# Optimization experiments

Hardware: AMD Instinct MI355X
Metric: run time of the kernel (lower is better)

The kernel has to match this reference:

```python
import jax, jax.numpy as jnp
import numpy as np

N_NODES = 50000
N_EDGES = 800000
D_IN = 788
D_HID = 256
N_REL = 7
N_CLS = 2


def rgcn_conv(x, w_rel, w_root, b, src, dst, edge_type):
    """PyG RGCNConv with default mean aggregation per relation + root weight + bias.
    x: (N, F_in); w_rel: (R, F_in, F_out); w_root: (F_in, F_out); b: (F_out,).
    src/dst: (E,) with edge_index[0]=source j, edge_index[1]=target i.
    """
    R, _, F_out = w_rel.shape
    N = x.shape[0]
    # transform-then-gather (equivalent to PyG's gather-then-transform, cheaper)
    x_rel = jnp.einsum('nf,rfo->rno', x, w_rel)          # (R, N, F_out)
    msg = x_rel[edge_type, src]                           # (E, F_out)
    agg = jnp.zeros((R, N, F_out), x.dtype).at[edge_type, dst].add(msg)
    cnt = jnp.zeros((R, N), x.dtype).at[edge_type, dst].add(1.0)
    out = (agg / jnp.clip(cnt, 1.0)[..., None]).sum(0)    # mean per relation, summed over relations
    return out + x @ w_root + b


def setup_inputs() -> dict:
    key = jax.random.key(0)
    ks = jax.random.split(key, 9)
    x = jax.random.normal(ks[0], (N_NODES, D_IN), dtype=jnp.float32)
    edge_index = jax.random.randint(ks[1], (2, N_EDGES), 0, N_NODES, dtype=jnp.int64)
    edge_type = jax.random.randint(ks[2], (N_EDGES,), 0, N_REL, dtype=jnp.int64)
    s1 = 0.05
    w1_rel = jax.random.normal(ks[3], (N_REL, D_IN, D_HID), dtype=jnp.float32) * s1
    w1_root = jax.random.normal(ks[4], (D_IN, D_HID), dtype=jnp.float32) * s1
    b1 = jnp.zeros((D_HID,), dtype=jnp.float32)
    w2_rel = jax.random.normal(ks[5], (N_REL, D_HID, N_CLS), dtype=jnp.float32) * s1
    w2_root = jax.random.normal(ks[6], (D_HID, N_CLS), dtype=jnp.float32) * s1
    b2 = jnp.zeros((N_CLS,), dtype=jnp.float32)
    return {"x": x, "edge_index": edge_index, "edge_type": edge_type,
            "w1_rel": w1_rel, "w1_root": w1_root, "b1": b1,
            "w2_rel": w2_rel, "w2_root": w2_root, "b2": b2}


def reference(x, edge_index, edge_type, w1_rel, w1_root, b1, w2_rel, w2_root, b2):
    src, dst = edge_index[0], edge_index[1]
    h = jax.nn.relu(rgcn_conv(x, w1_rel, w1_root, b1, src, dst, edge_type))
    # F.dropout(p=0.5) is identity in eval mode
    out = rgcn_conv(h, w2_rel, w2_root, b2, src, dst, edge_type)
    return out
```

## Files before the change

### kernel.cpp

```cpp
#include <hip/hip_runtime.h>
#include <hip/hip_bf16.h>
#include <stdint.h>

#define N_NODES 50000
#define N_EDGES 800000
#define D_IN    788
#define D_INP   800
#define D_HID   256
#define N_REL   7
#define NBINS   (N_REL * N_NODES)
#define NSCANB  342
#define NXTILE  391

typedef __attribute__((ext_vector_type(8))) short bf16x8;
typedef __attribute__((ext_vector_type(4))) float f32x4;
typedef __attribute__((ext_vector_type(4))) unsigned int u32x4;

__device__ __forceinline__ unsigned short f2bf(float f) {
  union { __hip_bfloat16 h; unsigned short u; } v;
  v.h = __float2bfloat16(f);
  return v.u;
}

__device__ __forceinline__ f32x4 bf4(ushort4 g) {
  union { unsigned int u; float f; } a, b, c, d;
  a.u = (unsigned)g.x << 16; b.u = (unsigned)g.y << 16;
  c.u = (unsigned)g.z << 16; d.u = (unsigned)g.w << 16;
  return (f32x4){a.f, b.f, c.f, d.f};
}

#define GLOAD16(g, l) __builtin_amdgcn_global_load_lds(                      \
    (const __attribute__((address_space(1))) unsigned int*)(g),              \
    (__attribute__((address_space(3))) unsigned int*)(l), 16, 0, 0)

__global__ void k_conv_w(const float* __restrict__ w_rel, const float* __restrict__ w_root,
                         unsigned short* __restrict__ wt) {
  int t = blockIdx.x * blockDim.x + threadIdx.x;
  if (t >= 8 * D_HID * 100) return;
  int m = t / (D_HID * 100);
  int rem = t % (D_HID * 100);
  int o = rem / 100, gi = rem % 100;
  int chunk = gi >> 2, p = gi & 3;
  int g = p ^ ((o >> 1) & 3);
  int k0 = chunk * 32 + g * 8;
  const float* src = (m < N_REL) ? (w_rel + (size_t)m * D_IN * D_HID) : w_root;
  union { unsigned short us[8]; u32x4 v; } pk;
#pragma unroll
  for (int j = 0; j < 8; j++)
    pk.us[j] = (k0 + j < D_IN) ? f2bf(src[(size_t)(k0 + j) * D_HID + o]) : (unsigned short)0;
  *(u32x4*)(wt + (size_t)(m * D_HID + o) * D_INP + chunk * 32 + p * 8) = pk.v;
}

__global__ void k_xbf(const float* __restrict__ x, unsigned short* __restrict__ xb) {
  int t = blockIdx.x * blockDim.x + threadIdx.x;
  if (t >= N_NODES * 100) return;
  int n = t / 100, gi = t % 100;
  int chunk = gi >> 2, p = gi & 3;
  int g = p ^ ((n >> 1) & 3);
  int c = chunk * 32 + g * 8;
  union { unsigned short us[8]; u32x4 v; } pk;
  if (c + 7 < D_IN) {
    float4 a = *(const float4*)(x + (size_t)n * D_IN + c);
    float4 b = *(const float4*)(x + (size_t)n * D_IN + c + 4);
    pk.us[0] = f2bf(a.x); pk.us[1] = f2bf(a.y); pk.us[2] = f2bf(a.z); pk.us[3] = f2bf(a.w);
    pk.us[4] = f2bf(b.x); pk.us[5] = f2bf(b.y); pk.us[6] = f2bf(b.z); pk.us[7] = f2bf(b.w);
  } else {
#pragma unroll
    for (int j = 0; j < 8; j++)
      pk.us[j] = (c + j < D_IN) ? f2bf(x[(size_t)n * D_IN + c + j]) : (unsigned short)0;
  }
  *(u32x4*)(xb + (size_t)n * D_INP + chunk * 32 + p * 8) = pk.v;
}

__global__ void k_count(const int* __restrict__ etype, const int* __restrict__ edst,
                        int* __restrict__ cnt) {
  int t = blockIdx.x * blockDim.x + threadIdx.x;
  if (t >= N_EDGES) return;
  atomicAdd(&cnt[etype[t] * N_NODES + edst[t]], 1);
}

__global__ void k_scan1(const int* __restrict__ cnt, int* __restrict__ bsum) {
  __shared__ int wsh[4];
  int b = blockIdx.x, tid = threadIdx.x;
  int base = b * 1024 + tid * 4;
  int4 v = {0, 0, 0, 0};
  if (base + 3 < NBINS) v = *(const int4*)(cnt + base);
  else { for (int i = 0; i < 4; i++) if (base + i < NBINS) ((int*)&v)[i] = cnt[base + i]; }
  int s = v.x + v.y + v.z + v.w;
  for (int o = 32; o > 0; o >>= 1) s += __shfl_down(s, o);
  if ((tid & 63) == 0) wsh[tid >> 6] = s;
  __syncthreads();
  if (tid == 0) bsum[b] = wsh[0] + wsh[1] + wsh[2] + wsh[3];
}

__global__ void k_scan2(const int* __restrict__ bsum, int* __restrict__ boff) {
  __shared__ int tmp[512];
  int tid = threadIdx.x;
  int mine = (tid < NSCANB) ? bsum[tid] : 0;
  tmp[tid] = mine;
  __syncthreads();
  for (int o = 1; o < 512; o <<= 1) {
    int v = (tid >= o) ? tmp[tid - o] : 0;
    __syncthreads();
    tmp[tid] += v;
    __syncthreads();
  }
  if (tid < NSCANB) boff[tid] = tmp[tid] - mine;
}

__global__ void k_scan3(const int* __restrict__ cnt, const int* __restrict__ boff,
                        int* __restrict__ S) {
  __shared__ int wsum[4];
  int b = blockIdx.x, tid = threadIdx.x;
  int base = b * 1024 + tid * 4;
  int4 v = {0, 0, 0, 0};
  if (base + 3 < NBINS) v = *(const int4*)(cnt + base);
  else { for (int i = 0; i < 4; i++) if (base + i < NBINS) ((int*)&v)[i] = cnt[base + i]; }
  int s = v.x + v.y + v.z + v.w;
  int lane = tid & 63, w = tid >> 6;
  int sc = s;
  for (int o = 1; o < 64; o <<= 1) { int u = __shfl_up(sc, o); if (lane >= o) sc += u; }
  if (lane == 63) wsum[w] = sc;
  __syncthreads();
  int wbase = 0;
  for (int i = 0; i < w; i++) wbase += wsum[i];
  int excl = boff[b] + wbase + sc - s;
  int o0 = excl, o1 = excl + v.x, o2 = o1 + v.y, o3 = o2 + v.z;
  if (base + 3 < NBINS) { int4 o4 = {o0, o1, o2, o3}; *(int4*)(S + base) = o4; }
  else {
    if (base     < NBINS) S[base]     = o0;
    if (base + 1 < NBINS) S[base + 1] = o1;
    if (base + 2 < NBINS) S[base + 2] = o2;
    if (base + 3 < NBINS) S[base + 3] = o3;
  }
}

__global__ void k_scatter(const int* __restrict__ etype, const int* __restrict__ edst,
                          const int* __restrict__ esrc, const int* __restrict__ S,
                          int* __restrict__ rank, int* __restrict__ psrc) {
  int t = blockIdx.x * blockDim.x + threadIdx.x;
  if (t >= N_EDGES) return;
  int bin = etype[t] * N_NODES + edst[t];
  int r = atomicAdd(&rank[bin], 1);
  psrc[S[bin] + r] = esrc[t];
}

template<int SWZ, int NMAT>
__global__ __launch_bounds__(512) void k_gemm_g(
    const unsigned short* __restrict__ xb, const unsigned short* __restrict__ wt,
    unsigned short* __restrict__ xrs, int mb) {
  __shared__ __align__(16) unsigned short As[128 * 32];
  __shared__ __align__(16) unsigned short Bs[256 * 32];

  int tid = threadIdx.x;
  int bx, by;
  if (SWZ) {
    int b = blockIdx.x;
    int l = (b % 8) * (NXTILE * NMAT / 8) + b / 8;
    bx = l / NMAT; by = l % NMAT;
  } else {
    bx = blockIdx.x; by = blockIdx.y;
  }
  int mat = mb + by;
  int m0 = bx * 128;
  const unsigned short* wsec = wt + (size_t)mat * (D_HID * D_INP);
  int lane = tid & 63, w = tid >> 6;
  int wm = w >> 2, wn = w & 3;

  int ar = tid >> 2;
  int arow = m0 + ar; if (arow > N_NODES - 1) arow = N_NODES - 1;
  const unsigned short* asrc = xb + (size_t)arow * D_INP + (tid & 3) * 8;
  const unsigned short* bsrc0 = wsec + (size_t)(tid >> 2) * D_INP + (tid & 3) * 8;
  const unsigned short* bsrc1 = bsrc0 + (size_t)128 * D_INP;
  unsigned short* al = As + tid * 8;
  unsigned short* bl0 = Bs + tid * 8;
  unsigned short* bl1 = Bs + 4096 + tid * 8;

  f32x4 acc[4][4];
#pragma unroll
  for (int i = 0; i < 4; i++)
#pragma unroll
    for (int j = 0; j < 4; j++) acc[i][j] = (f32x4){0.f, 0.f, 0.f, 0.f};

  int row = lane & 15, quad = lane >> 4;
  int rg = (quad ^ ((row >> 1) & 3)) * 8;

  for (int ks = 0; ks < 25; ks++) {
    int ko = ks * 32;
    GLOAD16(asrc + ko, al);
    GLOAD16(bsrc0 + ko, bl0);
    GLOAD16(bsrc1 + ko, bl1);
    __syncthreads();

    bf16x8 af[4], bfr[4];
#pragma unroll
    for (int i = 0; i < 4; i++)
      af[i] = *(const bf16x8*)(As + (wm * 64 + i * 16 + row) * 32 + rg);
#pragma unroll
    for (int j = 0; j < 4; j++)
      bfr[j] = *(const bf16x8*)(Bs + (wn * 64 + j * 16 + row) * 32 + rg);
#pragma unroll
    for (int i = 0; i < 4; i++)
#pragma unroll
      for (int j = 0; j < 4; j++)
        acc[i][j] = __builtin_amdgcn_mfma_f32_16x16x32_bf16(af[i], bfr[j], acc[i][j], 0, 0, 0);
    __syncthreads();
  }

  int col_l = lane & 15, rquad = lane >> 4;
  unsigned short* xo = xrs + (size_t)by * ((size_t)N_NODES * D_HID);
#pragma unroll
  for (int i = 0; i < 4; i++) {
#pragma unroll
    for (int reg = 0; reg < 4; reg++) {
      int node = m0 + wm * 64 + i * 16 + rquad * 4 + reg;
      if (node < N_NODES) {
#pragma unroll
        for (int j = 0; j < 4; j++)
          xo[(size_t)node * D_HID + wn * 64 + j * 16 + col_l] = f2bf(acc[i][j][reg]);
      }
    }
  }
}

__global__ __launch_bounds__(256) void k_gemm_f(
    const float* __restrict__ x, const unsigned short* __restrict__ wt,
    unsigned short* __restrict__ xrs, int mb) {
  __shared__ __align__(16) unsigned short As[64 * 40];
  __shared__ __align__(16) unsigned short Bs[256 * 40];

  int tid = threadIdx.x;
  int mat = mb + blockIdx.y;
  int m0 = blockIdx.x * 64;
  const unsigned short* wsec = wt + (size_t)mat * (D_HID * D_INP);
  int lane = tid & 63, w = tid >> 6;

  int ra = tid >> 2, ca = tid & 3, ca8 = ca * 8;
  int arow = m0 + ra; if (arow > N_NODES - 1) arow = N_NODES - 1;
  const float* apf = x + (size_t)arow * D_IN;
  const unsigned short* bgp = wsec + (size_t)ra * D_INP + (ca ^ ((ra >> 1) & 3)) * 8;
  unsigned short* al = As + ra * 40 + ca8;
  unsigned short* bl = Bs + ra * 40 + ca8;

  f32x4 acc[4][4];
#pragma unroll
  for (int i = 0; i < 4; i++)
#pragma unroll
    for (int j = 0; j < 4; j++) acc[i][j] = (f32x4){0.f, 0.f, 0.f, 0.f};

  float4 pa0 = *(const float4*)(apf + ca8);
  float4 pa1 = *(const float4*)(apf + ca8 + 4);
  u32x4 pb0 = *(const u32x4*)(bgp);
  u32x4 pb1 = *(const u32x4*)(bgp +  64 * D_INP);
  u32x4 pb2 = *(const u32x4*)(bgp + 128 * D_INP);
  u32x4 pb3 = *(const u32x4*)(bgp + 192 * D_INP);

  int row = lane & 15, quad = lane >> 4;
  for (int ks = 0; ks < 25; ks++) {
    if (ks < 24) {
      union { unsigned short us[8]; u32x4 v; } pk;
      pk.us[0] = f2bf(pa0.x); pk.us[1] = f2bf(pa0.y);
      pk.us[2] = f2bf(pa0.z); pk.us[3] = f2bf(pa0.w);
      pk.us[4] = f2bf(pa1.x); pk.us[5] = f2bf(pa1.y);
      pk.us[6] = f2bf(pa1.z); pk.us[7] = f2bf(pa1.w);
      *(u32x4*)al = pk.v;
    } else {
      float v0 = pa0.x, v1 = pa0.y, v2 = pa0.z, v3 = pa0.w;
      float v4 = pa1.x, v5 = pa1.y, v6 = pa1.z, v7 = pa1.w;
      if (ca8 == 16) { v0 = pa1.x; v1 = pa1.y; v2 = pa1.z; v3 = pa1.w;
                       v4 = 0.f; v5 = 0.f; v6 = 0.f; v7 = 0.f; }
      if (ca8 == 24) { v0 = 0.f; v1 = 0.f; v2 = 0.f; v3 = 0.f;
                       v4 = 0.f; v5 = 0.f; v6 = 0.f; v7 = 0.f; }
      union { unsigned short us[8]; u32x4 v; } pk;
      pk.us[0] = f2bf(v0); pk.us[1] = f2bf(v1); pk.us[2] = f2bf(v2); pk.us[3] = f2bf(v3);
      pk.us[4] = f2bf(v4); pk.us[5] = f2bf(v5); pk.us[6] = f2bf(v6); pk.us[7] = f2bf(v7);
      *(u32x4*)al = pk.v;
    }
    *(u32x4*)bl = pb0;
    *(u32x4*)(bl +  64 * 40) = pb1;
    *(u32x4*)(bl + 128 * 40) = pb2;
    *(u32x4*)(bl + 192 * 40) = pb3;
    __syncthreads();

    if (ks < 24) {
      int on = (ks + 1) * 32 + ca8;
      int lo = (on > 780) ? 780 : on;
      pa0 = *(const float4*)(apf + lo);
      pa1 = *(const float4*)(apf + lo + 4);
      int ko = (ks + 1) * 32;
      pb0 = *(const u32x4*)(bgp + ko);
      pb1 = *(const u32x4*)(bgp + ko +  64 * D_INP);
      pb2 = *(const u32x4*)(bgp + ko + 128 * D_INP);
      pb3 = *(const u32x4*)(bgp + ko + 192 * D_INP);
    }

    bf16x8 af[4], bfr[4];
#pragma unroll
    for (int i = 0; i < 4; i++)
      af[i] = *(const bf16x8*)(As + (i * 16 + row) * 40 + quad * 8);
#pragma unroll
    for (int j = 0; j < 4; j++)
      bfr[j] = *(const bf16x8*)(Bs + (w * 64 + j * 16 + row) * 40 + quad * 8);
#pragma unroll
    for (int i = 0; i < 4; i++)
#pragma unroll
      for (int j = 0; j < 4; j++)
        acc[i][j] = __builtin_amdgcn_mfma_f32_16x16x32_bf16(af[i], bfr[j], acc[i][j], 0, 0, 0);
    __syncthreads();
  }

  int col_l = lane & 15, rquad = lane >> 4;
  unsigned short* xo = xrs + (size_t)blockIdx.y * ((size_t)N_NODES * D_HID);
#pragma unroll
  for (int i = 0; i < 4; i++) {
#pragma unroll
    for (int reg = 0; reg < 4; reg++) {
      int node = m0 + i * 16 + rquad * 4 + reg;
      if (node < N_NODES) {
#pragma unroll
        for (int j = 0; j < 4; j++)
          xo[(size_t)node * D_HID + w * 64 + j * 16 + col_l] = f2bf(acc[i][j][reg]);
      }
    }
  }
}

__global__ __launch_bounds__(256) void k_agg8(
    const unsigned short* __restrict__ xrs, const int* __restrict__ S,
    const int* __restrict__ cnt, const int* __restrict__ psrc,
    const float* __restrict__ b1, const float* __restrict__ w2rel,
    const float* __restrict__ w2root, float* __restrict__ y) {
  int n = blockIdx.x * 4 + (threadIdx.x >> 6);
  int lane = threadIdx.x & 63;
  if (n >= N_NODES) return;

  int c_l = 0, p_l = 0;
  if (lane < N_REL) {
    c_l = cnt[lane * N_NODES + n];
    p_l = S[lane * N_NODES + n];
  }

  f32x4 acc = (f32x4){0.f, 0.f, 0.f, 0.f};
#pragma unroll
  for (int r = 0; r < N_REL; r++) {
    int c = __shfl(c_l, r);
    if (c > 0) {
      int p = __shfl(p_l, r);
      const unsigned short* slab = xrs + (size_t)r * N_NODES * D_HID;
      f32x4 s = (f32x4){0.f, 0.f, 0.f, 0.f};
      int e = 0;
      for (; e + 1 < c; e += 2) {
        int s0 = psrc[p + e], s1 = psrc[p + e + 1];
        ushort4 g0 = *(const ushort4*)(slab + (size_t)s0 * D_HID + lane * 4);
        ushort4 g1 = *(const ushort4*)(slab + (size_t)s1 * D_HID + lane * 4);
        s += bf4(g0) + bf4(g1);
      }
      if (e < c) {
        int s0 = psrc[p + e];
        ushort4 g0 = *(const ushort4*)(slab + (size_t)s0 * D_HID + lane * 4);
        s += bf4(g0);
      }
      acc += s * (1.0f / (float)c);
    }
  }

  ushort4 gr = *(const ushort4*)(xrs + ((size_t)7 * N_NODES + n) * D_HID + lane * 4);
  acc += bf4(gr);
  f32x4 b = *(const f32x4*)(b1 + lane * 4);
  f32x4 hv;
  hv[0] = fmaxf(acc[0] + b[0], 0.f);
  hv[1] = fmaxf(acc[1] + b[1], 0.f);
  hv[2] = fmaxf(acc[2] + b[2], 0.f);
  hv[3] = fmaxf(acc[3] + b[3], 0.f);

#pragma unroll
  for (int m = 0; m < 8; m++) {
    const float* wp = (m < N_REL) ? (w2rel + m * (D_HID * 2)) : w2root;
    f32x4 wa = *(const f32x4*)(wp + lane * 8);
    f32x4 wb = *(const f32x4*)(wp + lane * 8 + 4);
    float d0 = hv[0] * wa[0] + hv[1] * wa[2] + hv[2] * wb[0] + hv[3] * wb[2];
    float d1 = hv[0] * wa[1] + hv[1] * wa[3] + hv[2] * wb[1] + hv[3] * wb[3];
#pragma unroll
    for (int off = 32; off > 0; off >>= 1) {
      d0 += __shfl_down(d0, off);
      d1 += __shfl_down(d1, off);
    }
    if (lane == 0) {
      y[(size_t)m * (N_NODES * 2) + n * 2]     = d0;
      y[(size_t)m * (N_NODES * 2) + n * 2 + 1] = d1;
    }
  }
}

__global__ __launch_bounds__(256) void k_agg(
    const unsigned short* __restrict__ xrs, const int* __restrict__ S,
    const int* __restrict__ cnt, const int* __restrict__ psrc,
    float* __restrict__ h, const float* __restrict__ b1,
    const float* __restrict__ w2rel, const float* __restrict__ w2root,
    float* __restrict__ y, int r0, int pass) {
  int n = blockIdx.x * 4 + (threadIdx.x >> 6);
  int lane = threadIdx.x & 63;
  if (n >= N_NODES) return;
  f32x4 acc;
  if (pass == 0) acc = (f32x4){0.f, 0.f, 0.f, 0.f};
  else acc = *(const f32x4*)(h + (size_t)n * D_HID + lane * 4);

  int nr = (pass < 3) ? 2 : 1;
  for (int rr = 0; rr < nr; rr++) {
    int bin = (r0 + rr) * N_NODES + n;
    int c = cnt[bin];
    if (c > 0) {
      int p = S[bin];
      f32x4 s = (f32x4){0.f, 0.f, 0.f, 0.f};
      int e = 0;
      for (; e + 1 < c; e += 2) {
        int s0 = psrc[p + e], s1 = psrc[p + e + 1];
        ushort4 g0 = *(const ushort4*)(xrs + ((size_t)rr * N_NODES + s0) * D_HID + lane * 4);
        ushort4 g1 = *(const ushort4*)(xrs + ((size_t)rr * N_NODES + s1) * D_HID + lane * 4);
        s += bf4(g0) + bf4(g1);
      }
      if (e < c) {
        int s0 = psrc[p + e];
        ushort4 g0 = *(const ushort4*)(xrs + ((size_t)rr * N_NODES + s0) * D_HID + lane * 4);
        s += bf4(g0);
      }
      acc += s * (1.0f / (float)c);
    }
  }

  if (pass < 3) {
    *(f32x4*)(h + (size_t)n * D_HID + lane * 4) = acc;
    return;
  }

  ushort4 gr = *(const ushort4*)(xrs + ((size_t)1 * N_NODES + n) * D_HID + lane * 4);
  acc += bf4(gr);
  f32x4 b = *(const f32x4*)(b1 + lane * 4);
  f32x4 hv;
  hv[0] = fmaxf(acc[0] + b[0], 0.f);
  hv[1] = fmaxf(acc[1] + b[1], 0.f);
  hv[2] = fmaxf(acc[2] + b[2], 0.f);
  hv[3] = fmaxf(acc[3] + b[3], 0.f);

#pragma unroll
  for (int m = 0; m < 8; m++) {
    const float* wp = (m < N_REL) ? (w2rel + m * (D_HID * 2)) : w2root;
    f32x4 wa = *(const f32x4*)(wp + lane * 8);
    f32x4 wb = *(const f32x4*)(wp + lane * 8 + 4);
    float d0 = hv[0] * wa[0] + hv[1] * wa[2] + hv[2] * wb[0] + hv[3] * wb[2];
    float d1 = hv[0] * wa[1] + hv[1] * wa[3] + hv[2] * wb[1] + hv[3] * wb[3];
#pragma unroll
    for (int off = 32; off > 0; off >>= 1) {
      d0 += __shfl_down(d0, off);
      d1 += __shfl_down(d1, off);
    }
    if (lane == 0) {
      y[(size_t)m * (N_NODES * 2) + n * 2]     = d0;
      y[(size_t)m * (N_NODES * 2) + n * 2 + 1] = d1;
    }
  }
}

__global__ void k_out(const float* __restrict__ y, const float* __restrict__ b2,
                      const int* __restrict__ cnt, const int* __restrict__ S,
                      const int* __restrict__ psrc, float* __restrict__ out) {
  int t = blockIdx.x * blockDim.x + threadIdx.x;
  if (t < NBINS) {
    int c = cnt[t];
    if (c == 0) return;
    int p = S[t];
    int r = t / N_NODES;
    int i = t - r * N_NODES;
    const float* yr = y + (size_t)r * (N_NODES * 2);
    float s0 = 0.f, s1 = 0.f;
    for (int e = 0; e < c; e++) {
      int sc = psrc[p + e];
      float2 v = *(const float2*)(yr + sc * 2);
      s0 += v.x; s1 += v.y;
    }
    float is = 1.0f / (float)c;
    atomicAdd(out + (size_t)i * 2,     s0 * is);
    atomicAdd(out + (size_t)i * 2 + 1, s1 * is);
  } else if (t < NBINS + N_NODES) {
    int i = t - NBINS;
    float2 v = *(const float2*)(y + (size_t)N_REL * (N_NODES * 2) + i * 2);
    atomicAdd(out + (size_t)i * 2,     v.x + b2[0]);
    atomicAdd(out + (size_t)i * 2 + 1, v.y + b2[1]);
  }
}

#define OFF_WT   0u
#define OFF_XRS  3276800u
#define OFF_H    54476800u
#define OFF_CNT  105676800u
#define OFF_RANK 107076800u
#define OFF_S    108476800u
#define OFF_PSRC 109876800u
#define OFF_Y    113076800u
#define OFF_BSUM 116276800u
#define OFF_BOFF 116278848u
#define OFF_XB   116280896u
#define WS_NEED_XB 196280896ull

#define F_OFF_WT   0u
#define F_OFF_XRS  3276800u
#define F_OFF_CNT  208076800u
#define F_OFF_RANK 209476800u
#define F_OFF_S    210876800u
#define F_OFF_PSRC 212276800u
#define F_OFF_Y    215476800u
#define F_OFF_BSUM 218676800u
#define F_OFF_BOFF 218678848u
#define F_OFF_XB   218680896u
#define WS_NEED_FULL 298680896ull

extern "C" void kernel_launch(void* const* d_in, const int* in_sizes, int n_in,
                              void* d_out, int out_size, void* d_ws, size_t ws_size,
                              hipStream_t stream) {
  const float* x      = (const float*)d_in[0];
  const int*   eidx   = (const int*)d_in[1];
  const int*   etype  = (const int*)d_in[2];
  const float* w1rel  = (const float*)d_in[3];
  const float* w1root = (const float*)d_in[4];
  const float* b1     = (const float*)d_in[5];
  const float* w2rel  = (const float*)d_in[6];
  const float* w2root = (const float*)d_in[7];
  const float* b2     = (const float*)d_in[8];
  float* out = (float*)d_out;
  char* ws = (char*)d_ws;
  const int* esrc = eidx;
  const int* edst = eidx + N_EDGES;

  const bool full = (ws_size >= WS_NEED_FULL);
  const bool big  = !full && (ws_size >= WS_NEED_XB);

  hipMemsetAsync(d_out, 0, (size_t)out_size * sizeof(float), stream);

  if (full) {
    unsigned short* wt  = (unsigned short*)(ws + F_OFF_WT);
    unsigned short* xrs = (unsigned short*)(ws + F_OFF_XRS);
    int*   cnt  = (int*)(ws + F_OFF_CNT);
    int*   rank = (int*)(ws + F_OFF_RANK);
    int*   S    = (int*)(ws + F_OFF_S);
    int*   psrc = (int*)(ws + F_OFF_PSRC);
    float* y    = (float*)(ws + F_OFF_Y);
    int*   bsum = (int*)(ws + F_OFF_BSUM);
    int*   boff = (int*)(ws + F_OFF_BOFF);
    unsigned short* xb = (unsigned short*)(ws + F_OFF_XB);

    hipMemsetAsync(ws + F_OFF_CNT, 0, 2800000u, stream);

    k_conv_w<<<(8 * D_HID * 100 + 255) / 256, 256, 0, stream>>>(w1rel, w1root, wt);
    k_xbf<<<(N_NODES * 100 + 255) / 256, 256, 0, stream>>>(x, xb);
    k_count<<<(N_EDGES + 255) / 256, 256, 0, stream>>>(etype, edst, cnt);
    k_scan1<<<NSCANB, 256, 0, stream>>>(cnt, bsum);
    k_scan2<<<1, 512, 0, stream>>>(bsum, boff);
    k_scan3<<<NSCANB, 256, 0, stream>>>(cnt, boff, S);
    k_scatter<<<(N_EDGES + 255) / 256, 256, 0, stream>>>(etype, edst, esrc, S, rank, psrc);

    k_gemm_g<1, 8><<<NXTILE * 8, 512, 0, stream>>>(xb, wt, xrs, 0);
    k_agg8<<<(N_NODES + 3) / 4, 256, 0, stream>>>(xrs, S, cnt, psrc,
                                                  b1, w2rel, w2root, y);
    k_out<<<(NBINS + N_NODES + 255) / 256, 256, 0, stream>>>(y, b2, cnt, S, psrc, out);
    return;
  }

  unsigned short* wt  = (unsigned short*)(ws + OFF_WT);
  unsigned short* xrs = (unsigned short*)(ws + OFF_XRS);
  float* h    = (float*)(ws + OFF_H);
  int*   cnt  = (int*)(ws + OFF_CNT);
  int*   rank = (int*)(ws + OFF_RANK);
  int*   S    = (int*)(ws + OFF_S);
  int*   psrc = (int*)(ws + OFF_PSRC);
  float* y    = (float*)(ws + OFF_Y);
  int*   bsum = (int*)(ws + OFF_BSUM);
  int*   boff = (int*)(ws + OFF_BOFF);
  unsigned short* xb = (unsigned short*)(ws + OFF_XB);

  hipMemsetAsync(ws + OFF_CNT, 0, 2800000u, stream);

  k_conv_w<<<(8 * D_HID * 100 + 255) / 256, 256, 0, stream>>>(w1rel, w1root, wt);
  if (big)
    k_xbf<<<(N_NODES * 100 + 255) / 256, 256, 0, stream>>>(x, xb);
  k_count<<<(N_EDGES + 255) / 256, 256, 0, stream>>>(etype, edst, cnt);
  k_scan1<<<NSCANB, 256, 0, stream>>>(cnt, bsum);
  k_scan2<<<1, 512, 0, stream>>>(bsum, boff);
  k_scan3<<<NSCANB, 256, 0, stream>>>(cnt, boff, S);
  k_scatter<<<(N_EDGES + 255) / 256, 256, 0, stream>>>(etype, edst, esrc, S, rank, psrc);

  for (int p = 0; p < 4; p++) {
    if (big)
      k_gemm_g<0, 2><<<dim3(NXTILE, 2), 512, 0, stream>>>(xb, wt, xrs, 2 * p);
    else
      k_gemm_f<<<dim3(782, 2), 256, 0, stream>>>(x, wt, xrs, 2 * p);
    k_agg<<<(N_NODES + 3) / 4, 256, 0, stream>>>(xrs, S, cnt, psrc, h,
                                                 b1, w2rel, w2root, y, 2 * p, p);
  }

  k_out<<<(NBINS + N_NODES + 255) / 256, 256, 0, stream>>>(y, b2, cnt, S, psrc, out);
}
```

Before: 723.6 us.

## Split GEMM tiles to 128x128 with 256 threads and restructure layer-2 projection in agg8

The bf16 MFMA GEMM tile shrinks from 128x256 with 512 threads to 128x128 with 256 threads, doubling the block count and halving shared memory per block so more blocks fit per CU and the grid is spread more evenly. Each block now loads two A row groups and covers one half of the output columns. Separately, k_agg8 stages the hidden vector in shared memory so that each group of 8 lanes computes one of the 8 layer-2 projections. This replaces 8 full 64-lane shuffle reductions with one 3-step reduction. The trade-off is that A tiles are reloaded twice across the column halves.

Result: slower. 784.1 us (+8.4%).

```diff
diff --git a/kernel.cpp b/kernel.cpp
--- a/kernel.cpp
+++ b/kernel.cpp
@@ -145,36 +145,41 @@
   psrc[S[bin] + r] = esrc[t];
 }
 
-template<int SWZ, int NMAT>
-__global__ __launch_bounds__(512) void k_gemm_g(
+template<int SWZ, int NMATB>
+__global__ __launch_bounds__(256) void k_gemm_g(
     const unsigned short* __restrict__ xb, const unsigned short* __restrict__ wt,
     unsigned short* __restrict__ xrs, int mb) {
   __shared__ __align__(16) unsigned short As[128 * 32];
-  __shared__ __align__(16) unsigned short Bs[256 * 32];
+  __shared__ __align__(16) unsigned short Bs[128 * 32];
 
   int tid = threadIdx.x;
   int bx, by;
   if (SWZ) {
     int b = blockIdx.x;
-    int l = (b % 8) * (NXTILE * NMAT / 8) + b / 8;
-    bx = l / NMAT; by = l % NMAT;
+    int l = (b & 7) * ((NXTILE * NMATB * 2) >> 3) + (b >> 3);
+    bx = l / (NMATB * 2); by = l % (NMATB * 2);
   } else {
     bx = blockIdx.x; by = blockIdx.y;
   }
-  int mat = mb + by;
+  int mat = mb + (by >> 1);
+  int cb = by & 1;
   int m0 = bx * 128;
-  const unsigned short* wsec = wt + (size_t)mat * (D_HID * D_INP);
+  const unsigned short* wsec = wt + (size_t)mat * (D_HID * D_INP)
+                                  + (size_t)(cb * 128) * D_INP;
   int lane = tid & 63, w = tid >> 6;
-  int wm = w >> 2, wn = w & 3;
-
-  int ar = tid >> 2;
-  int arow = m0 + ar; if (arow > N_NODES - 1) arow = N_NODES - 1;
-  const unsigned short* asrc = xb + (size_t)arow * D_INP + (tid & 3) * 8;
-  const unsigned short* bsrc0 = wsec + (size_t)(tid >> 2) * D_INP + (tid & 3) * 8;
-  const unsigned short* bsrc1 = bsrc0 + (size_t)128 * D_INP;
-  unsigned short* al = As + tid * 8;
+  int wm = w >> 1, wn = w & 1;
+
+  int sr = tid >> 2, sg = (tid & 3) * 8;
+  int ar0 = m0 + sr;      if (ar0 > N_NODES - 1) ar0 = N_NODES - 1;
+  int ar1 = m0 + 64 + sr; if (ar1 > N_NODES - 1) ar1 = N_NODES - 1;
+  const unsigned short* asrc0 = xb + (size_t)ar0 * D_INP + sg;
+  const unsigned short* asrc1 = xb + (size_t)ar1 * D_INP + sg;
+  const unsigned short* bsrc0 = wsec + (size_t)sr * D_INP + sg;
+  const unsigned short* bsrc1 = bsrc0 + (size_t)64 * D_INP;
+  unsigned short* al0 = As + tid * 8;
+  unsigned short* al1 = As + 2048 + tid * 8;
   unsigned short* bl0 = Bs + tid * 8;
-  unsigned short* bl1 = Bs + 4096 + tid * 8;
+  unsigned short* bl1 = Bs + 2048 + tid * 8;
 
   f32x4 acc[4][4];
 #pragma unroll
@@ -187,7 +192,8 @@
 
   for (int ks = 0; ks < 25; ks++) {
     int ko = ks * 32;
-    GLOAD16(asrc + ko, al);
+    GLOAD16(asrc0 + ko, al0);
+    GLOAD16(asrc1 + ko, al1);
     GLOAD16(bsrc0 + ko, bl0);
     GLOAD16(bsrc1 + ko, bl1);
     __syncthreads();
@@ -208,7 +214,7 @@
   }
 
   int col_l = lane & 15, rquad = lane >> 4;
-  unsigned short* xo = xrs + (size_t)by * ((size_t)N_NODES * D_HID);
+  unsigned short* xo = xrs + (size_t)(by >> 1) * ((size_t)N_NODES * D_HID) + cb * 128;
 #pragma unroll
   for (int i = 0; i < 4; i++) {
 #pragma unroll
@@ -330,7 +336,9 @@
     const int* __restrict__ cnt, const int* __restrict__ psrc,
     const float* __restrict__ b1, const float* __restrict__ w2rel,
     const float* __restrict__ w2root, float* __restrict__ y) {
-  int n = blockIdx.x * 4 + (threadIdx.x >> 6);
+  __shared__ float hsh[4][256];
+  int wv = threadIdx.x >> 6;
+  int n = blockIdx.x * 4 + wv;
   int lane = threadIdx.x & 63;
   if (n >= N_NODES) return;
 
@@ -373,22 +381,27 @@
   hv[2] = fmaxf(acc[2] + b[2], 0.f);
   hv[3] = fmaxf(acc[3] + b[3], 0.f);
 
-#pragma unroll
-  for (int m = 0; m < 8; m++) {
-    const float* wp = (m < N_REL) ? (w2rel + m * (D_HID * 2)) : w2root;
-    f32x4 wa = *(const f32x4*)(wp + lane * 8);
-    f32x4 wb = *(const f32x4*)(wp + lane * 8 + 4);
-    float d0 = hv[0] * wa[0] + hv[1] * wa[2] + hv[2] * wb[0] + hv[3] * wb[2];
-    float d1 = hv[0] * wa[1] + hv[1] * wa[3] + hv[2] * wb[1] + hv[3] * wb[3];
-#pragma unroll
-    for (int off = 32; off > 0; off >>= 1) {
-      d0 += __shfl_down(d0, off);
-      d1 += __shfl_down(d1, off);
-    }
-    if (lane == 0) {
-      y[(size_t)m * (N_NODES * 2) + n * 2]     = d0;
-      y[(size_t)m * (N_NODES * 2) + n * 2 + 1] = d1;
-    }
+  *(f32x4*)&hsh[wv][lane * 4] = hv;
+  __builtin_amdgcn_wave_barrier();
+
+  int m = lane >> 3, sl = lane & 7;
+  const float* wp = (m < N_REL) ? (w2rel + m * (D_HID * 2)) : w2root;
+  int dbase = sl * 32;
+  float d0 = 0.f, d1 = 0.f;
+#pragma unroll
+  for (int dd = 0; dd < 8; dd++) {
+    f32x4 h4 = *(const f32x4*)&hsh[wv][dbase + dd * 4];
+    f32x4 wa = *(const f32x4*)(wp + (dbase + dd * 4) * 2);
+    f32x4 wb = *(const f32x4*)(wp + (dbase + dd * 4) * 2 + 4);
+    d0 += h4[0] * wa[0] + h4[1] * wa[2] + h4[2] * wb[0] + h4[3] * wb[2];
+    d1 += h4[0] * wa[1] + h4[1] * wa[3] + h4[2] * wb[1] + h4[3] * wb[3];
+  }
+  d0 += __shfl_down(d0, 1); d1 += __shfl_down(d1, 1);
+  d0 += __shfl_down(d0, 2); d1 += __shfl_down(d1, 2);
+  d0 += __shfl_down(d0, 4); d1 += __shfl_down(d1, 4);
+  if (sl == 0) {
+    y[(size_t)m * (N_NODES * 2) + n * 2]     = d0;
+    y[(size_t)m * (N_NODES * 2) + n * 2 + 1] = d1;
   }
 }
 
@@ -558,7 +571,7 @@
     k_scan3<<<NSCANB, 256, 0, stream>>>(cnt, boff, S);
     k_scatter<<<(N_EDGES + 255) / 256, 256, 0, stream>>>(etype, edst, esrc, S, rank, psrc);
 
-    k_gemm_g<1, 8><<<NXTILE * 8, 512, 0, stream>>>(xb, wt, xrs, 0);
+    k_gemm_g<1, 8><<<NXTILE * 16, 256, 0, stream>>>(xb, wt, xrs, 0);
     k_agg8<<<(N_NODES + 3) / 4, 256, 0, stream>>>(xrs, S, cnt, psrc,
                                                   b1, w2rel, w2root, y);
     k_out<<<(NBINS + N_NODES + 255) / 256, 256, 0, stream>>>(y, b2, cnt, S, psrc, out);
@@ -590,7 +603,7 @@
 
   for (int p = 0; p < 4; p++) {
     if (big)
-      k_gemm_g<0, 2><<<dim3(NXTILE, 2), 512, 0, stream>>>(xb, wt, xrs, 2 * p);
+      k_gemm_g<0, 2><<<dim3(NXTILE, 4), 256, 0, stream>>>(xb, wt, xrs, 2 * p);
     else
       k_gemm_f<<<dim3(782, 2), 256, 0, stream>>>(x, wt, xrs, 2 * p);
     k_agg<<<(N_NODES + 3) / 4, 256, 0, stream>>>(xrs, S, cnt, psrc, h,
```
